# Optimization experiments

Hardware: AMD Instinct MI355X
Metric: run time of the kernel (lower is better)

The kernel has to match this reference:

```python
import jax, jax.numpy as jnp
import numpy as np

B, C, H, W = 2, 64, 128, 128
HEADS = 8
HID = C  # hidden_size = dim in MHSA.__init__
EPS = 1e-12  # F.normalize default eps


def setup_inputs() -> dict:
    key = jax.random.key(0)
    ks = jax.random.split(key, 9)
    s = 0.05
    return {
        "x": jax.random.normal(ks[0], (B, C, H, W), jnp.float32),
        "W1": jax.random.normal(ks[1], (C, HID), jnp.float32) * s,
        "b1": jax.random.normal(ks[2], (C, HID), jnp.float32) * s,
        "W2": jax.random.normal(ks[3], (C, HID, HID), jnp.float32) * s,
        "b2": jax.random.normal(ks[4], (C, HID), jnp.float32) * s,
        "W3": jax.random.normal(ks[5], (C, HID, 3), jnp.float32) * s,
        "b3": jax.random.normal(ks[6], (C, 3), jnp.float32) * s,
        "temperature": jnp.ones((HEADS, 1, 1), jnp.float32),
        "Wout": jax.random.normal(ks[7], (C, C), jnp.float32) * s,  # [out, in] 1x1 conv
        "bout": jax.random.normal(ks[8], (C,), jnp.float32) * s,
    }


def reference(x, W1, b1, W2, b2, W3, b3, temperature, Wout, bout):
    b, c, h, w = x.shape
    # KAN QKV projection: per-channel tiny MLPs, batched over the channel axis.
    xt = jnp.transpose(x, (0, 2, 3, 1)).reshape(-1, c)          # [N, C]
    h1 = jax.nn.relu(xt[:, :, None] * W1[None] + b1[None])      # [N, C, HID]
    h2 = jax.nn.relu(jnp.einsum('nch,chk->nck', h1, W2) + b2[None])  # [N, C, HID]
    o = jnp.einsum('nch,cho->nco', h2, W3) + b3[None]           # [N, C, 3]
    # torch.cat of per-channel 3-col outputs along dim=1 == reshape [N, C*3]
    qkv = o.reshape(b, h, w, c * 3)
    qkv = jnp.transpose(qkv, (0, 3, 1, 2))                      # [b, 3c, h, w]
    q, k, v = jnp.split(qkv, 3, axis=1)                         # each [b, c, h, w]

    def to_heads(t):
        return t.reshape(b, HEADS, c // HEADS, h * w)

    q, k, v = to_heads(q), to_heads(k), to_heads(v)
    # L2-normalize along the spatial (last) axis, torch F.normalize semantics
    q = q / jnp.maximum(jnp.linalg.norm(q, axis=-1, keepdims=True), EPS)
    k = k / jnp.maximum(jnp.linalg.norm(k, axis=-1, keepdims=True), EPS)
    # Channel attention: [b, head, c_h, c_h]
    attn = jnp.einsum('bhcn,bhdn->bhcd', q, k) * temperature[None]
    attn = jax.nn.softmax(attn, axis=-1)
    out = jnp.einsum('bhcd,bhdn->bhcn', attn, v)                # [b, head, c_h, hw]
    out = out.reshape(b, c, h, w)
    # 1x1 conv projection
    out = jnp.einsum('bchw,oc->bohw', out, Wout) + bout[None, :, None, None]
    return out
```

## Files before the change

### kernel.cpp

```cpp
#include <hip/hip_runtime.h>
#include <hip/hip_bf16.h>
#include <math.h>

#define HW 16384
#define NCH 64

#define NG   2048
#define X0   (-8.0f)
#define INVDX 128.0f
#define DX   0.0078125f
#define PSTR (64*2048)

typedef __attribute__((ext_vector_type(8))) short s16x8;
typedef __attribute__((ext_vector_type(4))) short s16x4;
typedef __attribute__((ext_vector_type(2))) float f32x2;
typedef __attribute__((ext_vector_type(4))) float f32x4;
typedef __attribute__((ext_vector_type(8))) float f32x8;
typedef __attribute__((ext_vector_type(2))) __bf16 bf16x2;
typedef __attribute__((ext_vector_type(8))) __bf16 bf16x8;
typedef __attribute__((ext_vector_type(4))) unsigned u32x4;
typedef __attribute__((ext_vector_type(2))) unsigned u32x2;

__device__ __forceinline__ short bf16b(float f) {
    union { __hip_bfloat16 h; short s; } u;
    u.h = __float2bfloat16(f);
    return u.s;
}
__device__ __forceinline__ float bf2f(unsigned short us) {
    union { unsigned u; float f; } x;
    x.u = ((unsigned)us) << 16;
    return x.f;
}
__device__ __forceinline__ s16x8 cvt8(f32x8 v) {
    return __builtin_bit_cast(s16x8, __builtin_convertvector(v, bf16x8));
}
__device__ __forceinline__ unsigned pk_h1(f32x2 xw, f32x2 w, f32x2 b, f32x2 z2) {
    const f32x2 h = __builtin_elementwise_max(__builtin_elementwise_fma(xw, w, b), z2);
    return __builtin_bit_cast(unsigned, __builtin_convertvector(h, bf16x2));
}
__device__ __forceinline__ unsigned pk_relu_cvt(f32x2 v, f32x2 z2) {
    const f32x2 g = __builtin_elementwise_max(v, z2);
    return __builtin_bit_cast(unsigned, __builtin_convertvector(g, bf16x2));
}

#if __has_builtin(__builtin_amdgcn_mfma_f32_16x16x16bf16_1k)
#define HAVE_MFMA16 1
#else
#define HAVE_MFMA16 0
#endif

__global__ __launch_bounds__(64, 4) void kan_grid_mfma(
    const float* __restrict__ W1,
    const float* __restrict__ b1,
    const float* __restrict__ W2,
    const float* __restrict__ b2,
    const float* __restrict__ W3,
    const float* __restrict__ b3,
    float* __restrict__ table)
{
    const int c     = blockIdx.x & 63;
    const int chunk = blockIdx.x >> 6;
    const int lane  = threadIdx.x;
    const int l15   = lane & 15;
    const int grp   = lane >> 4;

    __shared__ float W2s[4096];
    __shared__ float W1s[64], B1s[64], B2s[64];
    {
        const float4* src = (const float4*)(W2 + c * 4096);
        float4* dst = (float4*)W2s;
        for (int i = lane; i < 1024; i += 64) dst[i] = src[i];
        W1s[lane] = W1[c*64 + lane];
        B1s[lane] = b1[c*64 + lane];
        B2s[lane] = b2[c*64 + lane];
    }
    __syncthreads();

    const float* W3c = W3 + c * 192;

    s16x8 a1[4][2];
#pragma unroll
    for (int m = 0; m < 4; ++m)
#pragma unroll
        for (int s = 0; s < 2; ++s) {
            f32x8 w;
#pragma unroll
            for (int jj = 0; jj < 8; ++jj)
                w[jj] = W2s[(s*32 + grp*8 + jj)*64 + m*16 + l15];
            a1[m][s] = cvt8(w);
        }

#if HAVE_MFMA16
    s16x4 a2[4];
#pragma unroll
    for (int m = 0; m < 4; ++m) {
        s16x4 f;
#pragma unroll
        for (int jj = 0; jj < 4; ++jj) {
            const int k = m*16 + grp*4 + jj;
            f[jj] = (l15 < 3) ? bf16b(W3c[k*3 + l15]) : (short)0;
        }
        a2[m] = f;
    }
    f32x4 b3r;
#pragma unroll
    for (int r = 0; r < 4; ++r) {
        const int row = grp*4 + r;
        b3r[r] = (row < 3) ? b3[c*3 + row] : 0.f;
    }
#else
    const float b3v0 = b3[c*3+0], b3v1 = b3[c*3+1], b3v2 = b3[c*3+2];
#endif

    float* Tq = table + c*NG;
    const char* b2base = (const char*)B2s;
    const f32x2 z2 = {0.f, 0.f};

    for (int t = 0; t < 8; ++t) {
        int z;
        asm volatile("v_mov_b32 %0, 0" : "=v"(z));

        const int pt = chunk*128 + t*16 + l15;
        const float xv = X0 + (float)pt * DX;
        const f32x2 xw = {xv, xv};

        s16x8 bf[2];
#pragma unroll
        for (int s = 0; s < 2; ++s) {
            const f32x4 w1lo = *(const f32x4*)&W1s[z + s*32 + grp*8];
            const f32x4 w1hi = *(const f32x4*)&W1s[z + s*32 + grp*8 + 4];
            const f32x4 b1lo = *(const f32x4*)&B1s[z + s*32 + grp*8];
            const f32x4 b1hi = *(const f32x4*)&B1s[z + s*32 + grp*8 + 4];
            u32x4 p;
            p[0] = pk_h1(xw, (f32x2){w1lo[0], w1lo[1]}, (f32x2){b1lo[0], b1lo[1]}, z2);
            p[1] = pk_h1(xw, (f32x2){w1lo[2], w1lo[3]}, (f32x2){b1lo[2], b1lo[3]}, z2);
            p[2] = pk_h1(xw, (f32x2){w1hi[0], w1hi[1]}, (f32x2){b1hi[0], b1hi[1]}, z2);
            p[3] = pk_h1(xw, (f32x2){w1hi[2], w1hi[3]}, (f32x2){b1hi[2], b1hi[3]}, z2);
            bf[s] = __builtin_bit_cast(s16x8, p);
        }

        f32x4 acc[4];
#pragma unroll
        for (int m = 0; m < 4; ++m) {
            acc[m] = *(const f32x4*)(b2base + (m*64 + grp*16 + z));
            acc[m] = __builtin_amdgcn_mfma_f32_16x16x32_bf16(a1[m][0], bf[0], acc[m], 0, 0, 0);
            acc[m] = __builtin_amdgcn_mfma_f32_16x16x32_bf16(a1[m][1], bf[1], acc[m], 0, 0, 0);
        }

#if HAVE_MFMA16
        s16x4 bb[4];
#pragma unroll
        for (int m = 0; m < 4; ++m) {
            u32x2 pv;
            pv[0] = pk_relu_cvt((f32x2){acc[m][0], acc[m][1]}, z2);
            pv[1] = pk_relu_cvt((f32x2){acc[m][2], acc[m][3]}, z2);
            bb[m] = __builtin_bit_cast(s16x4, pv);
        }
        f32x4 acc2a = b3r;
        f32x4 acc2b = {0.f, 0.f, 0.f, 0.f};
        acc2a = __builtin_amdgcn_mfma_f32_16x16x16bf16_1k(a2[0], bb[0], acc2a, 0, 0, 0);
        acc2b = __builtin_amdgcn_mfma_f32_16x16x16bf16_1k(a2[1], bb[1], acc2b, 0, 0, 0);
        acc2a = __builtin_amdgcn_mfma_f32_16x16x16bf16_1k(a2[2], bb[2], acc2a, 0, 0, 0);
        acc2b = __builtin_amdgcn_mfma_f32_16x16x16bf16_1k(a2[3], bb[3], acc2b, 0, 0, 0);
        if (grp == 0) {
            Tq[pt]          = acc2a[0] + acc2b[0];
            Tq[PSTR + pt]   = acc2a[1] + acc2b[1];
            Tq[2*PSTR + pt] = acc2a[2] + acc2b[2];
        }
#else
        float po0 = 0.f, po1 = 0.f, po2 = 0.f;
#pragma unroll
        for (int m = 0; m < 4; ++m)
#pragma unroll
            for (int r = 0; r < 4; ++r) {
                const float g = fmaxf(acc[m][r], 0.f);
                const int k = m*16 + grp*4 + r;
                po0 = fmaf(g, W3c[k*3+0], po0);
                po1 = fmaf(g, W3c[k*3+1], po1);
                po2 = fmaf(g, W3c[k*3+2], po2);
            }
        po0 += __shfl_xor(po0, 16, 64); po0 += __shfl_xor(po0, 32, 64);
        po1 += __shfl_xor(po1, 16, 64); po1 += __shfl_xor(po1, 32, 64);
        po2 += __shfl_xor(po2, 16, 64); po2 += __shfl_xor(po2, 32, 64);
        if (grp == 0) {
            Tq[pt]          = po0 + b3v0;
            Tq[PSTR + pt]   = po1 + b3v1;
            Tq[2*PSTR + pt] = po2 + b3v2;
        }
#endif
    }
}

__global__ __launch_bounds__(512) void gram_kernel(
    const float* __restrict__ x, const float* __restrict__ table,
    float* __restrict__ Dglob)
{
    const int bhd = blockIdx.x >> 5;
    const int spl = blockIdx.x & 31;
    const int b = bhd >> 3, hd = bhd & 7;
    const int tid = threadIdx.x;
    const int w   = tid >> 6;
    const int l   = tid & 63;
    const int grp = l >> 4;
    const int i16 = l & 15;
    const int ch  = i16 & 7;
    const int usek = i16 >> 3;

    __shared__ unsigned short T[2][8][NG];

    for (int e = tid; e < 8192; e += 512) {
        const int map = e >> 12;
        const int rem = e & 4095;
        const int c8  = rem >> 9;
        const int g   = rem & 511;
        const int gm  = map*64 + hd*8 + c8;
        const int cc  = gm / 3;
        const int jj  = gm % 3;
        const float4 v = ((const float4*)(table + jj*PSTR + cc*NG))[g];
        u32x2 pk;
        pk[0] = ((unsigned)(unsigned short)bf16b(v.x)) | (((unsigned)(unsigned short)bf16b(v.y)) << 16);
        pk[1] = ((unsigned)(unsigned short)bf16b(v.z)) | (((unsigned)(unsigned short)bf16b(v.w)) << 16);
        *(u32x2*)&T[map][c8][g*4] = pk;
    }
    __syncthreads();

    const unsigned short* Tc = T[usek][ch];
    const int gm = usek*64 + hd*8 + ch;
    const int cx = gm / 3;
    const float* xp = x + (b*NCH + cx)*HW + spl*512 + grp*8;

    f32x4 gacc = {0.f, 0.f, 0.f, 0.f};
#pragma unroll
    for (int s = 0; s < 2; ++s) {
        const int slab = w*2 + s;
        const float* xs = xp + slab*32;
        const f32x4 xlo = *(const f32x4*)xs;
        const f32x4 xhi = *(const f32x4*)(xs + 4);
        f32x8 vals;
#pragma unroll
        for (int e = 0; e < 8; ++e) {
            const float xv = (e < 4) ? xlo[e] : xhi[e-4];
            const float u = (xv - X0) * INVDX;
            int idx = (int)u;
            idx = min(max(idx, 0), NG - 2);
            const float fr = u - (float)idx;
            const float t0 = bf2f(Tc[idx]);
            const float t1 = bf2f(Tc[idx+1]);
            vals[e] = fmaf(fr, t1 - t0, t0);
        }
        const s16x8 frag = cvt8(vals);
        gacc = __builtin_amdgcn_mfma_f32_16x16x32_bf16(frag, frag, gacc, 0, 0, 0);
    }

    __syncthreads();
    float* red = (float*)&T[0][0][0];
#pragma unroll
    for (int r = 0; r < 4; ++r)
        red[w*256 + (grp*4 + r)*16 + i16] = gacc[r];
    __syncthreads();

    if (tid < 256) {
        const int row = tid >> 4, col = tid & 15;
        float g = 0.f;
#pragma unroll
        for (int ww = 0; ww < 8; ++ww) g += red[ww*256 + tid];
        int p = -1;
        if (row < 8 && col >= 8)        p = row*8 + (col - 8);
        else if (row == col && row < 8) p = 64 + row;
        else if (row == col)            p = 72 + (row - 8);
        if (p >= 0) atomicAdd(&Dglob[bhd*80 + p], g);
    }
}

__global__ __launch_bounds__(256) void v_eval(
    const float* __restrict__ x, const float* __restrict__ table,
    unsigned short* __restrict__ vbuf)
{
    const int m     = blockIdx.x >> 4;
    const int chunk = blockIdx.x & 15;
    const int t     = threadIdx.x;
    const int gm    = 128 + m;
    const int cx    = gm / 3;
    const int jj    = gm % 3;

    __shared__ float Lv[NG];
    const float4* Tv = (const float4*)(table + jj*PSTR + cx*NG);
    for (int i = t; i < NG/4; i += 256) ((float4*)Lv)[i] = Tv[i];
    __syncthreads();

    const int pxbase = chunk * 2048;
    const int b  = pxbase >> 14;
    const int hw = pxbase & 16383;
    const float* xr = x + (b*NCH + cx)*HW + hw;
    unsigned short* vr = vbuf + (b*NCH + m)*HW + hw;

    for (int i = 0; i < 4; ++i) {
        const int off = i*512 + t*2;
        const float2 xv = *(const float2*)(xr + off);
        float o[2];
#pragma unroll
        for (int e = 0; e < 2; ++e) {
            const float u = ((e ? xv.y : xv.x) - X0) * INVDX;
            int idx = (int)u;
            idx = min(max(idx, 0), NG - 2);
            const float fr = u - (float)idx;
            const float v0 = Lv[idx], v1 = Lv[idx+1];
            o[e] = fmaf(fr, v1 - v0, v0);
        }
        ushort2 vs;
        vs.x = (unsigned short)bf16b(o[0]);
        vs.y = (unsigned short)bf16b(o[1]);
        *(ushort2*)(vr + off) = vs;
    }
}

__global__ __launch_bounds__(256) void out_kernel(
    const unsigned short* __restrict__ vbuf, const float* __restrict__ Dglob,
    const float* __restrict__ temp, const float* __restrict__ Wout,
    const float* __restrict__ bout, float* __restrict__ out)
{
    const int b    = blockIdx.x >> 9;
    const int og   = (blockIdx.x >> 6) & 7;
    const int tile = blockIdx.x & 63;
    const int n = tile * 256 + threadIdx.x;
    const int t = threadIdx.x;

    __shared__ float D[8][80];
    __shared__ float attnS[8][8][8];
    __shared__ float2 AtS[64][4];

    for (int idx = t; idx < 640; idx += 256)
        ((float*)D)[idx] = Dglob[b*640 + idx];
    __syncthreads();

    if (t < 64) {
        const int hd = t >> 3, i = t & 7;
        const float invq = 1.f / fmaxf(sqrtf(D[hd][64+i]), 1e-12f);
        const float T = temp[hd];
        float l[8];
        float m = -1e30f;
#pragma unroll
        for (int j = 0; j < 8; ++j) {
            const float invk = 1.f / fmaxf(sqrtf(D[hd][72+j]), 1e-12f);
            l[j] = D[hd][i*8+j] * invq * invk * T;
            m = fmaxf(m, l[j]);
        }
        float s = 0.f;
#pragma unroll
        for (int j = 0; j < 8; ++j) { l[j] = expf(l[j] - m); s += l[j]; }
        const float inv = 1.f / s;
#pragma unroll
        for (int j = 0; j < 8; ++j) attnS[hd][i][j] = l[j] * inv;
    }
    __syncthreads();

    if (t < 128) {
        const int cv = t & 63, oq = t >> 6;
        const int hd = cv >> 3, jj = cv & 7;
        float res[4];
#pragma unroll
        for (int oo = 0; oo < 4; ++oo) {
            const int o = og*8 + oq*4 + oo;
            float s = 0.f;
#pragma unroll
            for (int i = 0; i < 8; ++i)
                s = fmaf(Wout[o*64 + hd*8 + i], attnS[hd][i][jj], s);
            res[oo] = s;
        }
        AtS[cv][oq*2 + 0] = make_float2(res[0], res[1]);
        AtS[cv][oq*2 + 1] = make_float2(res[2], res[3]);
    }
    __syncthreads();

    float acc[8];
#pragma unroll
    for (int o = 0; o < 8; ++o) acc[o] = 0.f;

    const unsigned short* vbase = vbuf + (b*NCH)*HW + n;
    for (int cv = 0; cv < 64; ++cv) {
        const float vv = bf2f(vbase[cv*HW]);
        const float2 w0 = AtS[cv][0];
        const float2 w1 = AtS[cv][1];
        const float2 w2 = AtS[cv][2];
        const float2 w3 = AtS[cv][3];
        acc[0] = fmaf(w0.x, vv, acc[0]);
        acc[1] = fmaf(w0.y, vv, acc[1]);
        acc[2] = fmaf(w1.x, vv, acc[2]);
        acc[3] = fmaf(w1.y, vv, acc[3]);
        acc[4] = fmaf(w2.x, vv, acc[4]);
        acc[5] = fmaf(w2.y, vv, acc[5]);
        acc[6] = fmaf(w3.x, vv, acc[6]);
        acc[7] = fmaf(w3.y, vv, acc[7]);
    }
#pragma unroll
    for (int o = 0; o < 8; ++o) {
        const int oc = og*8 + o;
        out[(b*NCH + oc)*HW + n] = acc[o] + bout[oc];
    }
}

extern "C" void kernel_launch(void* const* d_in, const int* in_sizes, int n_in,
                              void* d_out, int out_size, void* d_ws, size_t ws_size,
                              hipStream_t stream) {
    const float* x    = (const float*)d_in[0];
    const float* W1   = (const float*)d_in[1];
    const float* b1   = (const float*)d_in[2];
    const float* W2   = (const float*)d_in[3];
    const float* b2   = (const float*)d_in[4];
    const float* W3   = (const float*)d_in[5];
    const float* b3   = (const float*)d_in[6];
    const float* temp = (const float*)d_in[7];
    const float* Wout = (const float*)d_in[8];
    const float* bout = (const float*)d_in[9];
    float* out = (float*)d_out;

    float* ws = (float*)d_ws;
    float* table = ws;
    float* Dglob = ws + 393216;
    unsigned short* vbuf = (unsigned short*)(ws + 393216 + 1280);

    hipMemsetAsync(Dglob, 0, 1280 * sizeof(float), stream);
    kan_grid_mfma<<<1024, 64, 0, stream>>>(W1, b1, W2, b2, W3, b3, table);
    gram_kernel<<<512, 512, 0, stream>>>(x, table, Dglob);
    v_eval<<<1024, 256, 0, stream>>>(x, table, vbuf);
    out_kernel<<<1024, 256, 0, stream>>>(vbuf, Dglob, temp, Wout, bout, out);
}
```

Before: 51.98 us.

## Merge gram and V-eval kernels, prebuild bf16 table, drop memset launch

The table-building kernel now also writes a bf16 copy of the lookup table and zeroes the attention accumulator, which replaces the separate memset. The gram and V-evaluation kernels become one launch whose blocks split by index into the two roles. The gram blocks load the prebuilt bf16 table with 16-byte copies instead of converting from fp32. This removes two launches and the per-block conversion work, at the cost of an extra bf16 table write and a 64KB static shared allocation for every block, which may lower occupancy in the V-evaluation blocks.

```diff
diff --git a/kernel.cpp b/kernel.cpp
--- a/kernel.cpp
+++ b/kernel.cpp
@@ -56,13 +56,19 @@
     const float* __restrict__ b2,
     const float* __restrict__ W3,
     const float* __restrict__ b3,
-    float* __restrict__ table)
+    float* __restrict__ table,
+    unsigned short* __restrict__ tableBF,
+    float* __restrict__ Dglob)
 {
     const int c     = blockIdx.x & 63;
     const int chunk = blockIdx.x >> 6;
     const int lane  = threadIdx.x;
     const int l15   = lane & 15;
     const int grp   = lane >> 4;
+
+    if (blockIdx.x == 0) {
+        for (int i = lane; i < 1280; i += 64) Dglob[i] = 0.f;
+    }
 
     __shared__ float W2s[4096];
     __shared__ float W1s[64], B1s[64], B2s[64];
@@ -113,6 +119,7 @@
 #endif
 
     float* Tq = table + c*NG;
+    unsigned short* TqB = tableBF + c*NG;
     const char* b2base = (const char*)B2s;
     const f32x2 z2 = {0.f, 0.f};
 
@@ -163,9 +170,15 @@
         acc2a = __builtin_amdgcn_mfma_f32_16x16x16bf16_1k(a2[2], bb[2], acc2a, 0, 0, 0);
         acc2b = __builtin_amdgcn_mfma_f32_16x16x16bf16_1k(a2[3], bb[3], acc2b, 0, 0, 0);
         if (grp == 0) {
-            Tq[pt]          = acc2a[0] + acc2b[0];
-            Tq[PSTR + pt]   = acc2a[1] + acc2b[1];
-            Tq[2*PSTR + pt] = acc2a[2] + acc2b[2];
+            const float o0 = acc2a[0] + acc2b[0];
+            const float o1 = acc2a[1] + acc2b[1];
+            const float o2 = acc2a[2] + acc2b[2];
+            Tq[pt]          = o0;
+            Tq[PSTR + pt]   = o1;
+            Tq[2*PSTR + pt] = o2;
+            TqB[pt]          = (unsigned short)bf16b(o0);
+            TqB[PSTR + pt]   = (unsigned short)bf16b(o1);
+            TqB[2*PSTR + pt] = (unsigned short)bf16b(o2);
         }
 #else
         float po0 = 0.f, po1 = 0.f, po2 = 0.f;
@@ -183,134 +196,135 @@
         po1 += __shfl_xor(po1, 16, 64); po1 += __shfl_xor(po1, 32, 64);
         po2 += __shfl_xor(po2, 16, 64); po2 += __shfl_xor(po2, 32, 64);
         if (grp == 0) {
-            Tq[pt]          = po0 + b3v0;
-            Tq[PSTR + pt]   = po1 + b3v1;
-            Tq[2*PSTR + pt] = po2 + b3v2;
+            const float o0 = po0 + b3v0, o1 = po1 + b3v1, o2 = po2 + b3v2;
+            Tq[pt]          = o0;
+            Tq[PSTR + pt]   = o1;
+            Tq[2*PSTR + pt] = o2;
+            TqB[pt]          = (unsigned short)bf16b(o0);
+            TqB[PSTR + pt]   = (unsigned short)bf16b(o1);
+            TqB[2*PSTR + pt] = (unsigned short)bf16b(o2);
         }
 #endif
     }
 }
 
-__global__ __launch_bounds__(512) void gram_kernel(
+__global__ __launch_bounds__(512) void gram_v(
     const float* __restrict__ x, const float* __restrict__ table,
-    float* __restrict__ Dglob)
+    const unsigned short* __restrict__ tableBF,
+    float* __restrict__ Dglob, unsigned short* __restrict__ vbuf)
 {
-    const int bhd = blockIdx.x >> 5;
-    const int spl = blockIdx.x & 31;
-    const int b = bhd >> 3, hd = bhd & 7;
+    __shared__ __align__(16) unsigned char LB[65536];
+    const int bi  = blockIdx.x;
     const int tid = threadIdx.x;
-    const int w   = tid >> 6;
-    const int l   = tid & 63;
-    const int grp = l >> 4;
-    const int i16 = l & 15;
-    const int ch  = i16 & 7;
-    const int usek = i16 >> 3;
-
-    __shared__ unsigned short T[2][8][NG];
-
-    for (int e = tid; e < 8192; e += 512) {
-        const int map = e >> 12;
-        const int rem = e & 4095;
-        const int c8  = rem >> 9;
-        const int g   = rem & 511;
-        const int gm  = map*64 + hd*8 + c8;
-        const int cc  = gm / 3;
-        const int jj  = gm % 3;
-        const float4 v = ((const float4*)(table + jj*PSTR + cc*NG))[g];
-        u32x2 pk;
-        pk[0] = ((unsigned)(unsigned short)bf16b(v.x)) | (((unsigned)(unsigned short)bf16b(v.y)) << 16);
-        pk[1] = ((unsigned)(unsigned short)bf16b(v.z)) | (((unsigned)(unsigned short)bf16b(v.w)) << 16);
-        *(u32x2*)&T[map][c8][g*4] = pk;
-    }
-    __syncthreads();
-
-    const unsigned short* Tc = T[usek][ch];
-    const int gm = usek*64 + hd*8 + ch;
-    const int cx = gm / 3;
-    const float* xp = x + (b*NCH + cx)*HW + spl*512 + grp*8;
-
-    f32x4 gacc = {0.f, 0.f, 0.f, 0.f};
-#pragma unroll
-    for (int s = 0; s < 2; ++s) {
-        const int slab = w*2 + s;
-        const float* xs = xp + slab*32;
-        const f32x4 xlo = *(const f32x4*)xs;
-        const f32x4 xhi = *(const f32x4*)(xs + 4);
-        f32x8 vals;
-#pragma unroll
-        for (int e = 0; e < 8; ++e) {
-            const float xv = (e < 4) ? xlo[e] : xhi[e-4];
-            const float u = (xv - X0) * INVDX;
-            int idx = (int)u;
-            idx = min(max(idx, 0), NG - 2);
-            const float fr = u - (float)idx;
-            const float t0 = bf2f(Tc[idx]);
-            const float t1 = bf2f(Tc[idx+1]);
-            vals[e] = fmaf(fr, t1 - t0, t0);
-        }
-        const s16x8 frag = cvt8(vals);
-        gacc = __builtin_amdgcn_mfma_f32_16x16x32_bf16(frag, frag, gacc, 0, 0, 0);
-    }
-
-    __syncthreads();
-    float* red = (float*)&T[0][0][0];
-#pragma unroll
-    for (int r = 0; r < 4; ++r)
-        red[w*256 + (grp*4 + r)*16 + i16] = gacc[r];
-    __syncthreads();
-
-    if (tid < 256) {
-        const int row = tid >> 4, col = tid & 15;
-        float g = 0.f;
-#pragma unroll
-        for (int ww = 0; ww < 8; ++ww) g += red[ww*256 + tid];
-        int p = -1;
-        if (row < 8 && col >= 8)        p = row*8 + (col - 8);
-        else if (row == col && row < 8) p = 64 + row;
-        else if (row == col)            p = 72 + (row - 8);
-        if (p >= 0) atomicAdd(&Dglob[bhd*80 + p], g);
-    }
-}
-
-__global__ __launch_bounds__(256) void v_eval(
-    const float* __restrict__ x, const float* __restrict__ table,
-    unsigned short* __restrict__ vbuf)
-{
-    const int m     = blockIdx.x >> 4;
-    const int chunk = blockIdx.x & 15;
-    const int t     = threadIdx.x;
-    const int gm    = 128 + m;
-    const int cx    = gm / 3;
-    const int jj    = gm % 3;
-
-    __shared__ float Lv[NG];
-    const float4* Tv = (const float4*)(table + jj*PSTR + cx*NG);
-    for (int i = t; i < NG/4; i += 256) ((float4*)Lv)[i] = Tv[i];
-    __syncthreads();
-
-    const int pxbase = chunk * 2048;
-    const int b  = pxbase >> 14;
-    const int hw = pxbase & 16383;
-    const float* xr = x + (b*NCH + cx)*HW + hw;
-    unsigned short* vr = vbuf + (b*NCH + m)*HW + hw;
-
-    for (int i = 0; i < 4; ++i) {
-        const int off = i*512 + t*2;
-        const float2 xv = *(const float2*)(xr + off);
-        float o[2];
-#pragma unroll
-        for (int e = 0; e < 2; ++e) {
-            const float u = ((e ? xv.y : xv.x) - X0) * INVDX;
-            int idx = (int)u;
-            idx = min(max(idx, 0), NG - 2);
-            const float fr = u - (float)idx;
-            const float v0 = Lv[idx], v1 = Lv[idx+1];
-            o[e] = fmaf(fr, v1 - v0, v0);
-        }
-        ushort2 vs;
-        vs.x = (unsigned short)bf16b(o[0]);
-        vs.y = (unsigned short)bf16b(o[1]);
-        *(ushort2*)(vr + off) = vs;
+
+    if (bi < 512) {
+        const int bhd = bi >> 5;
+        const int spl = bi & 31;
+        const int b = bhd >> 3, hd = bhd & 7;
+        const int w   = tid >> 6;
+        const int l   = tid & 63;
+        const int grp = l >> 4;
+        const int i16 = l & 15;
+        const int ch  = i16 & 7;
+        const int usek = i16 >> 3;
+
+        unsigned short* T = (unsigned short*)LB;
+
+        for (int e = tid; e < 4096; e += 512) {
+            const int map = e >> 11;
+            const int rem = e & 2047;
+            const int c8  = rem >> 8;
+            const int g   = rem & 255;
+            const int gm  = map*64 + hd*8 + c8;
+            const int cc  = gm / 3;
+            const int jj  = gm % 3;
+            const u32x4 v = ((const u32x4*)(tableBF + jj*PSTR + cc*NG))[g];
+            *(u32x4*)&T[(map*8 + c8)*NG + g*8] = v;
+        }
+        __syncthreads();
+
+        const unsigned short* Tc = &T[(usek*8 + ch)*NG];
+        const int gm = usek*64 + hd*8 + ch;
+        const int cx = gm / 3;
+        const float* xp = x + (b*NCH + cx)*HW + spl*512 + grp*8;
+
+        f32x4 gacc = {0.f, 0.f, 0.f, 0.f};
+#pragma unroll
+        for (int s = 0; s < 2; ++s) {
+            const int slab = w*2 + s;
+            const float* xs = xp + slab*32;
+            const f32x4 xlo = *(const f32x4*)xs;
+            const f32x4 xhi = *(const f32x4*)(xs + 4);
+            f32x8 vals;
+#pragma unroll
+            for (int e = 0; e < 8; ++e) {
+                const float xv = (e < 4) ? xlo[e] : xhi[e-4];
+                const float u = (xv - X0) * INVDX;
+                int idx = (int)u;
+                idx = min(max(idx, 0), NG - 2);
+                const float fr = u - (float)idx;
+                const float t0 = bf2f(Tc[idx]);
+                const float t1 = bf2f(Tc[idx+1]);
+                vals[e] = fmaf(fr, t1 - t0, t0);
+            }
+            const s16x8 frag = cvt8(vals);
+            gacc = __builtin_amdgcn_mfma_f32_16x16x32_bf16(frag, frag, gacc, 0, 0, 0);
+        }
+
+        __syncthreads();
+        float* red = (float*)LB;
+#pragma unroll
+        for (int r = 0; r < 4; ++r)
+            red[w*256 + (grp*4 + r)*16 + i16] = gacc[r];
+        __syncthreads();
+
+        if (tid < 256) {
+            const int row = tid >> 4, col = tid & 15;
+            float g = 0.f;
+#pragma unroll
+            for (int ww = 0; ww < 8; ++ww) g += red[ww*256 + tid];
+            int p = -1;
+            if (row < 8 && col >= 8)        p = row*8 + (col - 8);
+            else if (row == col && row < 8) p = 64 + row;
+            else if (row == col)            p = 72 + (row - 8);
+            if (p >= 0) atomicAdd(&Dglob[bhd*80 + p], g);
+        }
+    } else {
+        const int bi2   = bi - 512;
+        const int m     = bi2 >> 3;
+        const int chunk = bi2 & 7;
+        const int gm    = 128 + m;
+        const int cx    = gm / 3;
+        const int jj    = gm % 3;
+
+        float* Lv = (float*)LB;
+        ((float4*)Lv)[tid] = ((const float4*)(table + jj*PSTR + cx*NG))[tid];
+        __syncthreads();
+
+        const int pxbase = chunk * 4096;
+        const int b  = pxbase >> 14;
+        const int hw = pxbase & 16383;
+        const float* xr = x + (b*NCH + cx)*HW + hw;
+        unsigned short* vr = vbuf + (b*NCH + m)*HW + hw;
+
+        for (int i = 0; i < 4; ++i) {
+            const int off = i*1024 + tid*2;
+            const float2 xv = *(const float2*)(xr + off);
+            float o[2];
+#pragma unroll
+            for (int e = 0; e < 2; ++e) {
+                const float u = ((e ? xv.y : xv.x) - X0) * INVDX;
+                int idx = (int)u;
+                idx = min(max(idx, 0), NG - 2);
+                const float fr = u - (float)idx;
+                const float v0 = Lv[idx], v1 = Lv[idx+1];
+                o[e] = fmaf(fr, v1 - v0, v0);
+            }
+            ushort2 vs;
+            vs.x = (unsigned short)bf16b(o[0]);
+            vs.y = (unsigned short)bf16b(o[1]);
+            *(ushort2*)(vr + off) = vs;
+        }
     }
 }
 
@@ -416,12 +430,11 @@
 
     float* ws = (float*)d_ws;
     float* table = ws;
-    float* Dglob = ws + 393216;
-    unsigned short* vbuf = (unsigned short*)(ws + 393216 + 1280);
-
-    hipMemsetAsync(Dglob, 0, 1280 * sizeof(float), stream);
-    kan_grid_mfma<<<1024, 64, 0, stream>>>(W1, b1, W2, b2, W3, b3, table);
-    gram_kernel<<<512, 512, 0, stream>>>(x, table, Dglob);
-    v_eval<<<1024, 256, 0, stream>>>(x, table, vbuf);
+    unsigned short* tableBF = (unsigned short*)(ws + 393216);
+    float* Dglob = ws + 393216 + 196608;
+    unsigned short* vbuf = (unsigned short*)(ws + 393216 + 196608 + 1280);
+
+    kan_grid_mfma<<<1024, 64, 0, stream>>>(W1, b1, W2, b2, W3, b3, table, tableBF, Dglob);
+    gram_v<<<1024, 512, 0, stream>>>(x, table, tableBF, Dglob, vbuf);
     out_kernel<<<1024, 256, 0, stream>>>(vbuf, Dglob, temp, Wout, bout, out);
 }
```

New measurement: 43.89 us. 1.18x faster.
